# Performance work log

Measured on AMD Instinct MI355X. Metric: run time of the kernel, lower is better.

The kernel has to match this reference:

```python
import jax, jax.numpy as jnp
import numpy as np

V, H, E, B, T = 32000, 1024, 512, 32, 64
EPS = 1e-5


def setup_inputs() -> dict:
    key = jax.random.key(0)
    ks = jax.random.split(key, 12)
    s = 0.05
    return {
        'image_feat': jax.random.normal(ks[0], (B, 2048), jnp.float32),
        'captions': jax.random.randint(ks[1], (B, T), 0, V, jnp.int64)
            if jax.config.jax_enable_x64 else jax.random.randint(ks[1], (B, T), 0, V, jnp.int32),
        'lin_W': jax.random.normal(ks[2], (E, 2048), jnp.float32) * s,
        'lin_b': jnp.zeros((E,), jnp.float32),
        'bn_gamma': jnp.ones((E,), jnp.float32),
        'bn_beta': jnp.zeros((E,), jnp.float32),
        'emb': jax.random.normal(ks[3], (V, E), jnp.float32) * s,
        'lstm_Wih0': jax.random.normal(ks[4], (4 * H, E), jnp.float32) * s,
        'lstm_Whh0': jax.random.normal(ks[5], (4 * H, H), jnp.float32) * s,
        'lstm_bih0': jnp.zeros((4 * H,), jnp.float32),
        'lstm_bhh0': jnp.zeros((4 * H,), jnp.float32),
        'lstm_Wih1': jax.random.normal(ks[6], (4 * H, H), jnp.float32) * s,
        'lstm_Whh1': jax.random.normal(ks[7], (4 * H, H), jnp.float32) * s,
        'lstm_bih1': jnp.zeros((4 * H,), jnp.float32),
        'lstm_bhh1': jnp.zeros((4 * H,), jnp.float32),
        'fc_W': jax.random.normal(ks[8], (V, H), jnp.float32) * s,
        'fc_b': jnp.zeros((V,), jnp.float32),
    }


def _lstm_layer(xs, Wih, Whh, bih, bhh):
    # xs: (B, T, in) -> hs: (B, T, H). PyTorch gate order i,f,g,o.
    b, t, _ = xs.shape
    h_dim = Whh.shape[1]
    pre = jnp.einsum('bti,gi->btg', xs, Wih) + bih + bhh  # input part for all steps

    def step(carry, p):
        h, c = carry
        g = p + h @ Whh.T
        i, f, gg, o = jnp.split(g, 4, axis=-1)
        c = jax.nn.sigmoid(f) * c + jax.nn.sigmoid(i) * jnp.tanh(gg)
        h = jax.nn.sigmoid(o) * jnp.tanh(c)
        return (h, c), h

    h0 = jnp.zeros((b, h_dim), xs.dtype)
    (_, _), hs = jax.lax.scan(step, (h0, h0), jnp.swapaxes(pre, 0, 1))
    return jnp.swapaxes(hs, 0, 1)


def reference(image_feat, captions, lin_W, lin_b, bn_gamma, bn_beta, emb,
              lstm_Wih0, lstm_Whh0, lstm_bih0, lstm_bhh0,
              lstm_Wih1, lstm_Whh1, lstm_bih1, lstm_bhh1, fc_W, fc_b):
    # image embed: Linear + BatchNorm1d (training-mode batch stats)
    x = image_feat @ lin_W.T + lin_b  # (B, E)
    mu = jnp.mean(x, axis=0)
    var = jnp.var(x, axis=0)
    x = bn_gamma * (x - mu) * jax.lax.rsqrt(var + EPS) + bn_beta

    # teacher-forced decode: step0 = image embed, steps 1..T-1 = caption embeds
    cap_emb = emb[captions[:, :-1]]  # (B, T-1, E)
    xs = jnp.concatenate([x[:, None, :], cap_emb], axis=1)  # (B, T, E)

    hs = _lstm_layer(xs, lstm_Wih0, lstm_Whh0, lstm_bih0, lstm_bhh0)
    hs = _lstm_layer(hs, lstm_Wih1, lstm_Whh1, lstm_bih1, lstm_bhh1)

    return jnp.einsum('bth,vh->btv', hs, fc_W) + fc_b  # (B, T, V)
```

## Files before the change

### kernel.cpp

```cpp
#include <hip/hip_runtime.h>

typedef __bf16 bf16;
typedef __attribute__((ext_vector_type(4))) float floatx4;
typedef __attribute__((ext_vector_type(8))) bf16 bf16x8;
typedef __attribute__((ext_vector_type(4))) bf16 bf16x4;
typedef __attribute__((ext_vector_type(4))) unsigned uintx4;
typedef __attribute__((ext_vector_type(2))) unsigned uintx2;

typedef const __attribute__((address_space(1))) void gconst_t;
typedef __attribute__((address_space(3))) void lds_t;

__device__ __forceinline__ void load_lds16(const void* g, void* l) {
  __builtin_amdgcn_global_load_lds((gconst_t*)g, (lds_t*)l, 16, 0, 0);
}

__device__ __forceinline__ float sigm(float x) { return 1.f / (1.f + __expf(-x)); }
__device__ __forceinline__ float tanh_f(float x) { return 2.f / (1.f + __expf(-2.f * x)) - 1.f; }

__device__ __forceinline__ void st_coh_u32(void* p, unsigned v) {
  asm volatile("global_store_dword %0, %1, off sc0 sc1" :: "v"(p), "v"(v) : "memory");
}
__device__ __forceinline__ void st_coh_u128(void* p, uintx4 v) {
  asm volatile("global_store_dwordx4 %0, %1, off sc0 sc1" :: "v"(p), "v"(v) : "memory");
}
__device__ __forceinline__ uintx2 ld_coh_u32x2(const void* p) {
  uintx2 r;
  asm volatile("global_load_dwordx2 %0, %1, off sc0 sc1\n\ts_waitcnt vmcnt(0)"
               : "=v"(r) : "v"(p) : "memory");
  return r;
}

__global__ void k_cvt(const float* __restrict__ in, bf16* __restrict__ out, int n4) {
  int i = blockIdx.x * 256 + threadIdx.x;
  if (i < n4) {
    float4 v = ((const float4*)in)[i];
    bf16x4 u = { (bf16)v.x, (bf16)v.y, (bf16)v.z, (bf16)v.w };
    ((bf16x4*)out)[i] = u;
  }
}

__global__ void k_bias_sum(const float* __restrict__ a, const float* __restrict__ b,
                           float* __restrict__ o, int n) {
  int i = blockIdx.x * 256 + threadIdx.x;
  if (i < n) o[i] = a[i] + b[i];
}

__global__ void k_zero(unsigned* __restrict__ p) {
  p[threadIdx.x] = 0u;
}

__global__ __launch_bounds__(256) void k_linbn(
    const float* __restrict__ img, const float* __restrict__ W,
    const float* __restrict__ lb, const float* __restrict__ gamma,
    const float* __restrict__ beta, bf16* __restrict__ xs)
{
  const int e = blockIdx.x;
  const int wave = threadIdx.x >> 6, lane = threadIdx.x & 63;
  __shared__ float sums[32];
  const float* wrow = W + (size_t)e * 2048;
  for (int b = wave; b < 32; b += 4) {
    const float* irow = img + (size_t)b * 2048;
    float s = 0.f;
#pragma unroll
    for (int j = 0; j < 8; ++j) {
      const int k = j * 256 + lane * 4;
      float4 a = *(const float4*)(irow + k);
      float4 w = *(const float4*)(wrow + k);
      s += a.x * w.x + a.y * w.y + a.z * w.z + a.w * w.w;
    }
#pragma unroll
    for (int off = 32; off > 0; off >>= 1) s += __shfl_down(s, off);
    if (lane == 0) sums[b] = s + lb[e];
  }
  __syncthreads();
  if (threadIdx.x < 32) {
    const float x = sums[threadIdx.x];
    float m = x, m2 = x * x;
#pragma unroll
    for (int mask = 16; mask > 0; mask >>= 1) {
      m  += __shfl_xor(m, mask);
      m2 += __shfl_xor(m2, mask);
    }
    m *= (1.f / 32.f); m2 *= (1.f / 32.f);
    const float var = m2 - m * m;
    const float xn = gamma[e] * (x - m) * rsqrtf(var + 1e-5f) + beta[e];
    xs[(size_t)threadIdx.x * 64 * 512 + e] = (bf16)xn;
  }
}

__global__ void k_embed(const int* __restrict__ cap, const float* __restrict__ emb,
                        bf16* __restrict__ xs)
{
  const int blk = blockIdx.x;
  const int b = blk / 63, j = blk % 63;
  const int tok = cap[b * 64 + j];
  const float* src = emb + (size_t)tok * 512;
  bf16* dst = xs + ((size_t)b * 64 + j + 1) * 512;
  float4 v = ((const float4*)src)[threadIdx.x];
  bf16x4 u = { (bf16)v.x, (bf16)v.y, (bf16)v.z, (bf16)v.w };
  *(bf16x4*)(dst + threadIdx.x * 4) = u;
}

__global__ __launch_bounds__(256) void k_gemm(
    const bf16* __restrict__ A, const float* __restrict__ Bt,
    const float* __restrict__ bias, float* __restrict__ C,
    int K, int N)
{
  __shared__ bf16 lA[128 * 32];
  __shared__ bf16 lB[128 * 32];
  const int tid = threadIdx.x;
  const int lane = tid & 63;
  const int wm = ((tid >> 6) >> 1) * 64;
  const int wn = ((tid >> 6) & 1) * 64;
  const int nwg = gridDim.x * gridDim.y;
  int wg = blockIdx.y * gridDim.x + blockIdx.x;
  wg = (wg & 7) * (nwg >> 3) + (wg >> 3);
  const size_t row0 = (size_t)(wg & 15) * 128;
  const size_t col0 = (size_t)(wg >> 4) * 128;
  floatx4 acc[4][4] = {};
  const bf16*  aSrc = A  + (row0 + (tid >> 2)) * (size_t)K + (tid & 3) * 8;
  const float* bSrc = Bt + (col0 + (tid >> 3)) * (size_t)K + (tid & 7) * 4;
  char* lAb = (char*)&lA[0];

  for (int k0 = 0; k0 < K; k0 += 32) {
    __syncthreads();
#pragma unroll
    for (int s = 0; s < 2; ++s)
      load_lds16(aSrc + (size_t)s * 64 * K + k0, lAb + s * 4096 + tid * 16);
#pragma unroll
    for (int s = 0; s < 4; ++s) {
      float4 v = *(const float4*)(bSrc + (size_t)s * 32 * K + k0);
      bf16x4 u = { (bf16)v.x, (bf16)v.y, (bf16)v.z, (bf16)v.w };
      *(bf16x4*)&lB[(s * 32 + (tid >> 3)) * 32 + (tid & 7) * 4] = u;
    }
    __syncthreads();
    bf16x8 af[4], bfv[4];
#pragma unroll
    for (int i = 0; i < 4; ++i)
      af[i] = *(const bf16x8*)&lA[(wm + i * 16 + (lane & 15)) * 32 + (lane >> 4) * 8];
#pragma unroll
    for (int j = 0; j < 4; ++j)
      bfv[j] = *(const bf16x8*)&lB[(wn + j * 16 + (lane & 15)) * 32 + (lane >> 4) * 8];
#pragma unroll
    for (int i = 0; i < 4; ++i)
#pragma unroll
      for (int j = 0; j < 4; ++j)
        acc[i][j] = __builtin_amdgcn_mfma_f32_16x16x32_bf16(af[i], bfv[j], acc[i][j], 0, 0, 0);
  }
#pragma unroll
  for (int i = 0; i < 4; ++i)
#pragma unroll
    for (int j = 0; j < 4; ++j)
#pragma unroll
      for (int r = 0; r < 4; ++r) {
        const size_t row = row0 + wm + i * 16 + (lane >> 4) * 4 + r;
        const size_t col = col0 + wn + j * 16 + (lane & 15);
        C[row * (size_t)N + col] = acc[i][j][r] + bias[col];
      }
}

__global__ __launch_bounds__(256) void k_gemm_bf(
    const bf16* __restrict__ A, const bf16* __restrict__ B,
    const float* __restrict__ bias, float* __restrict__ C,
    int K, int N)
{
  __shared__ bf16 lA[128 * 32];
  __shared__ bf16 lB[128 * 32];
  const int tid = threadIdx.x;
  const int lane = tid & 63;
  const int wm = ((tid >> 6) >> 1) * 64;
  const int wn = ((tid >> 6) & 1) * 64;
  const int nwg = gridDim.x * gridDim.y;
  int wg = blockIdx.y * gridDim.x + blockIdx.x;
  wg = (wg & 7) * (nwg >> 3) + (wg >> 3);
  const size_t row0 = (size_t)(wg & 15) * 128;
  const size_t col0 = (size_t)(wg >> 4) * 128;
  floatx4 acc[4][4] = {};
  const bf16* aSrc = A + (row0 + (tid >> 2)) * (size_t)K + (tid & 3) * 8;
  const bf16* bSrc = B + (col0 + (tid >> 2)) * (size_t)K + (tid & 3) * 8;
  char* lAb = (char*)&lA[0];
  char* lBb = (char*)&lB[0];

  for (int k0 = 0; k0 < K; k0 += 32) {
    __syncthreads();
#pragma unroll
    for (int s = 0; s < 2; ++s) {
      load_lds16(aSrc + (size_t)s * 64 * K + k0, lAb + s * 4096 + tid * 16);
      load_lds16(bSrc + (size_t)s * 64 * K + k0, lBb + s * 4096 + tid * 16);
    }
    __syncthreads();
    bf16x8 af[4], bfv[4];
#pragma unroll
    for (int i = 0; i < 4; ++i)
      af[i] = *(const bf16x8*)&lA[(wm + i * 16 + (lane & 15)) * 32 + (lane >> 4) * 8];
#pragma unroll
    for (int j = 0; j < 4; ++j)
      bfv[j] = *(const bf16x8*)&lB[(wn + j * 16 + (lane & 15)) * 32 + (lane >> 4) * 8];
#pragma unroll
    for (int i = 0; i < 4; ++i)
#pragma unroll
      for (int j = 0; j < 4; ++j)
        acc[i][j] = __builtin_amdgcn_mfma_f32_16x16x32_bf16(af[i], bfv[j], acc[i][j], 0, 0, 0);
  }
#pragma unroll
  for (int i = 0; i < 4; ++i)
#pragma unroll
    for (int j = 0; j < 4; ++j)
#pragma unroll
      for (int r = 0; r < 4; ++r) {
        const size_t row = row0 + wm + i * 16 + (lane >> 4) * 4 + r;
        const size_t col = col0 + wn + j * 16 + (lane & 15);
        C[row * (size_t)N + col] = acc[i][j][r] + bias[col];
      }
}

__device__ __forceinline__ void wait_flags(const unsigned* flags, unsigned tgt) {
  const int lane = threadIdx.x & 63;
  const unsigned* p = flags + 2 * lane;
  int spins = 0;
  for (;;) {
    uintx2 f = ld_coh_u32x2(p);
    if (__all(f.x >= tgt && f.y >= tgt)) break;
    if (++spins > 50000) break;
    __builtin_amdgcn_s_sleep(1);
  }
  asm volatile("" ::: "memory");
}

__global__ __launch_bounds__(256) void k_lstm_scan(
    bf16* __restrict__ hs, const float* __restrict__ pre,
    const bf16* __restrict__ whh, unsigned* __restrict__ flags)
{
  __shared__ bf16 lW[32 * 1024];
  __shared__ bf16 hstage[32][8];
  const int tid  = threadIdx.x;
  const int lane = tid & 63;
  const int wave = tid >> 6;
  const int tn   = wave >> 1;
  const int tb   = wave & 1;
  const int n0   = blockIdx.x * 8;

#pragma unroll
  for (int it = 0; it < 16; ++it) {
    const int idx  = it * 256 + tid;
    const int r    = idx >> 7;
    const int c16  = idx & 127;
    const int grow = (r & 3) * 1024 + n0 + (r >> 2);
    const bf16x8 v = *(const bf16x8*)(whh + (size_t)grow * 1024 + c16 * 8);
    int byte = r * 2048 + c16 * 16;
    byte ^= (r & 7) << 4;
    *(bf16x8*)((char*)lW + byte) = v;
  }
  __syncthreads();

  const int arow  = tn * 16 + (lane & 15);
  const int axor  = (arow & 7) << 4;
  const int abase = arow * 2048 + (lane >> 4) * 16;
  const int brow  = tb * 16 + (lane & 15);
  const int cown  = tn * 4 + (lane >> 4);
  const char* lWb = (const char*)lW;

  float cstate = 0.f;
  const float* preb = pre + (size_t)brow * 64 * 4096 + (n0 + cown);
  const bf16* hr = hs + (size_t)brow * 65536 + (lane >> 4) * 8;
  bf16* hwrow = hs + (size_t)tid * 65536 + n0;

#pragma unroll 1
  for (int t = 0; t < 64; ++t) {
    const float* pp = preb + (size_t)t * 4096;
    float g0 = pp[0], g1 = pp[1024], g2 = pp[2048], g3 = pp[3072];
    if (t > 0) {
      if (wave == 0) wait_flags(flags, (unsigned)t);
      __syncthreads();
      const bf16* hp = hr + (size_t)(t - 1) * 1024;
      floatx4 acc0 = {}, acc1 = {};
#pragma unroll
      for (int kk = 0; kk < 32; kk += 2) {
        const bf16x8 a0 = *(const bf16x8*)(lWb + ((abase + kk * 64) ^ axor));
        const bf16x8 b0 = *(const bf16x8*)(hp + kk * 32);
        acc0 = __builtin_amdgcn_mfma_f32_16x16x32_bf16(a0, b0, acc0, 0, 0, 0);
        const bf16x8 a1 = *(const bf16x8*)(lWb + ((abase + kk * 64 + 64) ^ axor));
        const bf16x8 b1 = *(const bf16x8*)(hp + kk * 32 + 32);
        acc1 = __builtin_amdgcn_mfma_f32_16x16x32_bf16(a1, b1, acc1, 0, 0, 0);
      }
      g0 += acc0[0] + acc1[0];
      g1 += acc0[1] + acc1[1];
      g2 += acc0[2] + acc1[2];
      g3 += acc0[3] + acc1[3];
    }
    const float iv = sigm(g0), fv = sigm(g1), gv = tanh_f(g2), ov = sigm(g3);
    cstate = fv * cstate + iv * gv;
    hstage[brow][cown] = (bf16)(ov * tanh_f(cstate));
    __syncthreads();
    if (tid < 32) {
      const uintx4 hv = *(const uintx4*)&hstage[tid][0];
      st_coh_u128(hwrow + (size_t)t * 1024, hv);
      asm volatile("s_waitcnt vmcnt(0)" ::: "memory");
    }
    __syncthreads();
    if (tid == 0)
      st_coh_u32(flags + blockIdx.x, (unsigned)(t + 1));
  }
}

extern "C" void kernel_launch(void* const* d_in, const int* in_sizes, int n_in,
                              void* d_out, int out_size, void* d_ws, size_t ws_size,
                              hipStream_t stream)
{
  const float* image = (const float*)d_in[0];
  const int*   caps  = (const int*)d_in[1];
  const float* linW  = (const float*)d_in[2];
  const float* linb  = (const float*)d_in[3];
  const float* gamma = (const float*)d_in[4];
  const float* beta  = (const float*)d_in[5];
  const float* emb   = (const float*)d_in[6];
  const float* Wih0  = (const float*)d_in[7];
  const float* Whh0  = (const float*)d_in[8];
  const float* bih0  = (const float*)d_in[9];
  const float* bhh0  = (const float*)d_in[10];
  const float* Wih1  = (const float*)d_in[11];
  const float* Whh1  = (const float*)d_in[12];
  const float* bih1  = (const float*)d_in[13];
  const float* bhh1  = (const float*)d_in[14];
  const float* fcW   = (const float*)d_in[15];
  const float* fcb   = (const float*)d_in[16];
  float* out = (float*)d_out;

  char* ws = (char*)d_ws;
  size_t off = 0;
  auto alloc = [&](size_t bytes) {
    char* p = ws + off;
    off += (bytes + 255) & ~(size_t)255;
    return p;
  };
  bf16*  whh0b = (bf16*)alloc(4096ull * 1024 * 2);
  bf16*  whh1b = (bf16*)alloc(4096ull * 1024 * 2);
  bf16*  xsb   = (bf16*)alloc(2048ull * 512 * 2);
  bf16*  hs0b  = (bf16*)alloc(2048ull * 1024 * 2);
  bf16*  hs1b  = (bf16*)alloc(2048ull * 1024 * 2);
  float* pre   = (float*)alloc(2048ull * 4096 * 4);
  float* bsum0 = (float*)alloc(4096 * 4);
  float* bsum1 = (float*)alloc(4096 * 4);
  unsigned* flg = (unsigned*)alloc(1024);
  const bool big = ws_size >= ((size_t)127 << 20);
  bf16* fcwb = big ? (bf16*)alloc(32000ull * 1024 * 2) : (bf16*)0;

  k_zero<<<1, 256, 0, stream>>>(flg);
  k_cvt<<<4096, 256, 0, stream>>>(Whh0, whh0b, 4096 * 1024 / 4);
  k_cvt<<<4096, 256, 0, stream>>>(Whh1, whh1b, 4096 * 1024 / 4);
  if (big) k_cvt<<<32000, 256, 0, stream>>>(fcW, fcwb, 32000 * 1024 / 4);
  k_bias_sum<<<16, 256, 0, stream>>>(bih0, bhh0, bsum0, 4096);
  k_bias_sum<<<16, 256, 0, stream>>>(bih1, bhh1, bsum1, 4096);
  k_linbn<<<512, 256, 0, stream>>>(image, linW, linb, gamma, beta, xsb);
  k_embed<<<2016, 128, 0, stream>>>(caps, emb, xsb);

  k_gemm<<<dim3(16, 32), 256, 0, stream>>>(xsb, Wih0, bsum0, pre, 512, 4096);
  k_lstm_scan<<<128, 256, 0, stream>>>(hs0b, pre, whh0b, flg);
  k_gemm<<<dim3(16, 32), 256, 0, stream>>>(hs0b, Wih1, bsum1, pre, 1024, 4096);
  k_lstm_scan<<<128, 256, 0, stream>>>(hs1b, pre, whh1b, flg + 128);
  if (big)
    k_gemm_bf<<<dim3(16, 250), 256, 0, stream>>>(hs1b, fcwb, fcb, out, 1024, 32000);
  else
    k_gemm<<<dim3(16, 250), 256, 0, stream>>>(hs1b, fcW, fcb, out, 1024, 32000);

  (void)in_sizes; (void)n_in; (void)out_size; (void)ws_size;
}
```

Baseline: 1.476 ms.

## Fuse both LSTM layers into one wavefront-pipelined persistent kernel

Result: slower. 1.553 ms (+5.2%).

```diff
diff --git a/kernel.cpp b/kernel.cpp
--- a/kernel.cpp
+++ b/kernel.cpp
@@ -26,6 +26,12 @@
 __device__ __forceinline__ uintx2 ld_coh_u32x2(const void* p) {
   uintx2 r;
   asm volatile("global_load_dwordx2 %0, %1, off sc0 sc1\n\ts_waitcnt vmcnt(0)"
+               : "=v"(r) : "v"(p) : "memory");
+  return r;
+}
+__device__ __forceinline__ uintx4 ld_coh_u32x4(const void* p) {
+  uintx4 r;
+  asm volatile("global_load_dwordx4 %0, %1, off sc0 sc1\n\ts_waitcnt vmcnt(0)"
                : "=v"(r) : "v"(p) : "memory");
   return r;
 }
@@ -214,43 +220,83 @@
       }
 }
 
-__device__ __forceinline__ void wait_flags(const unsigned* flags, unsigned tgt) {
+__device__ __forceinline__ void stage_w(const bf16* __restrict__ w, int n0,
+                                        char* ldsbase, int tid) {
+#pragma unroll
+  for (int it = 0; it < 16; ++it) {
+    const int idx  = it * 256 + tid;
+    const int r    = idx >> 7;
+    const int c16  = idx & 127;
+    const int grow = (r & 3) * 1024 + n0 + (r >> 2);
+    const bf16x8 v = *(const bf16x8*)(w + (size_t)grow * 1024 + c16 * 8);
+    int byte = r * 2048 + c16 * 16;
+    byte ^= (r & 7) << 4;
+    *(bf16x8*)(ldsbase + byte) = v;
+  }
+}
+
+__device__ __forceinline__ void gemv_pass(const char* lWb, int abase, int axor,
+                                          const bf16* hp, floatx4& acc0, floatx4& acc1) {
+#pragma unroll
+  for (int g8 = 0; g8 < 4; ++g8) {
+    bf16x8 hb[8];
+#pragma unroll
+    for (int u = 0; u < 8; ++u)
+      hb[u] = *(const bf16x8*)(hp + (g8 * 8 + u) * 32);
+#pragma unroll
+    for (int u = 0; u < 8; ++u) {
+      const bf16x8 a = *(const bf16x8*)(lWb + ((abase + (g8 * 8 + u) * 64) ^ axor));
+      if (u & 1) acc1 = __builtin_amdgcn_mfma_f32_16x16x32_bf16(a, hb[u], acc1, 0, 0, 0);
+      else       acc0 = __builtin_amdgcn_mfma_f32_16x16x32_bf16(a, hb[u], acc0, 0, 0, 0);
+    }
+  }
+}
+
+__device__ __forceinline__ void poll128(const unsigned* flags, unsigned tgt) {
   const int lane = threadIdx.x & 63;
   const unsigned* p = flags + 2 * lane;
   int spins = 0;
   for (;;) {
     uintx2 f = ld_coh_u32x2(p);
     if (__all(f.x >= tgt && f.y >= tgt)) break;
-    if (++spins > 50000) break;
+    if (++spins > 20000) break;
     __builtin_amdgcn_s_sleep(1);
   }
   asm volatile("" ::: "memory");
 }
 
-__global__ __launch_bounds__(256) void k_lstm_scan(
-    bf16* __restrict__ hs, const float* __restrict__ pre,
-    const bf16* __restrict__ whh, unsigned* __restrict__ flags)
-{
-  __shared__ bf16 lW[32 * 1024];
+__device__ __forceinline__ void poll256(const unsigned* flags, unsigned tgt0, unsigned tgt1) {
+  const int lane = threadIdx.x & 63;
+  const unsigned tgt = (lane < 32) ? tgt0 : tgt1;
+  const unsigned* p = flags + 4 * lane;
+  int spins = 0;
+  for (;;) {
+    uintx4 f = ld_coh_u32x4(p);
+    if (__all(f.x >= tgt && f.y >= tgt && f.z >= tgt && f.w >= tgt)) break;
+    if (++spins > 20000) break;
+    __builtin_amdgcn_s_sleep(1);
+  }
+  asm volatile("" ::: "memory");
+}
+
+__global__ __launch_bounds__(256, 1) void k_lstm_fused(
+    bf16* __restrict__ hs0, bf16* __restrict__ hs1,
+    const float* __restrict__ pre0, const float* __restrict__ bs1,
+    const bf16* __restrict__ whh0, const bf16* __restrict__ whh1,
+    const bf16* __restrict__ wih1, unsigned* __restrict__ flags)
+{
+  __shared__ bf16 lW[2][32 * 1024];
   __shared__ bf16 hstage[32][8];
   const int tid  = threadIdx.x;
   const int lane = tid & 63;
   const int wave = tid >> 6;
-  const int tn   = wave >> 1;
-  const int tb   = wave & 1;
-  const int n0   = blockIdx.x * 8;
-
-#pragma unroll
-  for (int it = 0; it < 16; ++it) {
-    const int idx  = it * 256 + tid;
-    const int r    = idx >> 7;
-    const int c16  = idx & 127;
-    const int grow = (r & 3) * 1024 + n0 + (r >> 2);
-    const bf16x8 v = *(const bf16x8*)(whh + (size_t)grow * 1024 + c16 * 8);
-    int byte = r * 2048 + c16 * 16;
-    byte ^= (r & 7) << 4;
-    *(bf16x8*)((char*)lW + byte) = v;
-  }
+  const bool l1  = blockIdx.x >= 128;
+  const int blk  = l1 ? (int)blockIdx.x - 128 : (int)blockIdx.x;
+  const int n0   = blk * 8;
+  const int tn   = wave >> 1, tb = wave & 1;
+
+  stage_w(l1 ? whh1 : whh0, n0, (char*)&lW[0][0], tid);
+  if (l1) stage_w(wih1, n0, (char*)&lW[1][0], tid);
   __syncthreads();
 
   const int arow  = tn * 16 + (lane & 15);
@@ -258,35 +304,47 @@
   const int abase = arow * 2048 + (lane >> 4) * 16;
   const int brow  = tb * 16 + (lane & 15);
   const int cown  = tn * 4 + (lane >> 4);
-  const char* lWb = (const char*)lW;
+  const char* lWhh = (const char*)&lW[0][0];
+  const char* lWih = (const char*)&lW[1][0];
+
+  float b0g = 0.f, b1g = 0.f, b2g = 0.f, b3g = 0.f;
+  if (l1) {
+    b0g = bs1[0 * 1024 + n0 + cown];
+    b1g = bs1[1 * 1024 + n0 + cown];
+    b2g = bs1[2 * 1024 + n0 + cown];
+    b3g = bs1[3 * 1024 + n0 + cown];
+  }
+
+  bf16* hw = l1 ? hs1 : hs0;
+  bf16* hwrow = hw + (size_t)tid * 65536 + n0;
+  const bf16* hr_own = hw  + (size_t)brow * 65536 + (lane >> 4) * 8;
+  const bf16* hr_h0  = hs0 + (size_t)brow * 65536 + (lane >> 4) * 8;
+  const float* preb  = pre0 + (size_t)brow * 64 * 4096 + (n0 + cown);
+  unsigned* myflag = flags + (l1 ? 128 : 0) + blk;
 
   float cstate = 0.f;
-  const float* preb = pre + (size_t)brow * 64 * 4096 + (n0 + cown);
-  const bf16* hr = hs + (size_t)brow * 65536 + (lane >> 4) * 8;
-  bf16* hwrow = hs + (size_t)tid * 65536 + n0;
-
 #pragma unroll 1
   for (int t = 0; t < 64; ++t) {
-    const float* pp = preb + (size_t)t * 4096;
-    float g0 = pp[0], g1 = pp[1024], g2 = pp[2048], g3 = pp[3072];
-    if (t > 0) {
-      if (wave == 0) wait_flags(flags, (unsigned)t);
+    float g0, g1, g2, g3;
+    floatx4 acc0 = {}, acc1 = {};
+    if (!l1) {
+      const float* pp = preb + (size_t)t * 4096;
+      g0 = pp[0]; g1 = pp[1024]; g2 = pp[2048]; g3 = pp[3072];
+      if (t > 0) {
+        if (wave == 0) poll128(flags, (unsigned)t);
+        __syncthreads();
+        gemv_pass(lWhh, abase, axor, hr_own + (size_t)(t - 1) * 1024, acc0, acc1);
+      }
+      g0 += acc0[0] + acc1[0]; g1 += acc0[1] + acc1[1];
+      g2 += acc0[2] + acc1[2]; g3 += acc0[3] + acc1[3];
+    } else {
+      if (wave == 0) poll256(flags, (unsigned)(t + 1), (unsigned)t);
       __syncthreads();
-      const bf16* hp = hr + (size_t)(t - 1) * 1024;
-      floatx4 acc0 = {}, acc1 = {};
-#pragma unroll
-      for (int kk = 0; kk < 32; kk += 2) {
-        const bf16x8 a0 = *(const bf16x8*)(lWb + ((abase + kk * 64) ^ axor));
-        const bf16x8 b0 = *(const bf16x8*)(hp + kk * 32);
-        acc0 = __builtin_amdgcn_mfma_f32_16x16x32_bf16(a0, b0, acc0, 0, 0, 0);
-        const bf16x8 a1 = *(const bf16x8*)(lWb + ((abase + kk * 64 + 64) ^ axor));
-        const bf16x8 b1 = *(const bf16x8*)(hp + kk * 32 + 32);
-        acc1 = __builtin_amdgcn_mfma_f32_16x16x32_bf16(a1, b1, acc1, 0, 0, 0);
-      }
-      g0 += acc0[0] + acc1[0];
-      g1 += acc0[1] + acc1[1];
-      g2 += acc0[2] + acc1[2];
-      g3 += acc0[3] + acc1[3];
+      gemv_pass(lWih, abase, axor, hr_h0 + (size_t)t * 1024, acc0, acc1);
+      if (t > 0)
+        gemv_pass(lWhh, abase, axor, hr_own + (size_t)(t - 1) * 1024, acc0, acc1);
+      g0 = b0g + acc0[0] + acc1[0]; g1 = b1g + acc0[1] + acc1[1];
+      g2 = b2g + acc0[2] + acc1[2]; g3 = b3g + acc0[3] + acc1[3];
     }
     const float iv = sigm(g0), fv = sigm(g1), gv = tanh_f(g2), ov = sigm(g3);
     cstate = fv * cstate + iv * gv;
@@ -296,10 +354,8 @@
       const uintx4 hv = *(const uintx4*)&hstage[tid][0];
       st_coh_u128(hwrow + (size_t)t * 1024, hv);
       asm volatile("s_waitcnt vmcnt(0)" ::: "memory");
-    }
-    __syncthreads();
-    if (tid == 0)
-      st_coh_u32(flags + blockIdx.x, (unsigned)(t + 1));
+      if (tid == 0) st_coh_u32(myflag, (unsigned)(t + 1));
+    }
   }
 }
 
@@ -335,6 +391,7 @@
   };
   bf16*  whh0b = (bf16*)alloc(4096ull * 1024 * 2);
   bf16*  whh1b = (bf16*)alloc(4096ull * 1024 * 2);
+  bf16*  wih1b = (bf16*)alloc(4096ull * 1024 * 2);
   bf16*  xsb   = (bf16*)alloc(2048ull * 512 * 2);
   bf16*  hs0b  = (bf16*)alloc(2048ull * 1024 * 2);
   bf16*  hs1b  = (bf16*)alloc(2048ull * 1024 * 2);
@@ -342,12 +399,13 @@
   float* bsum0 = (float*)alloc(4096 * 4);
   float* bsum1 = (float*)alloc(4096 * 4);
   unsigned* flg = (unsigned*)alloc(1024);
-  const bool big = ws_size >= ((size_t)127 << 20);
+  const bool big = ws_size >= ((size_t)136 << 20);
   bf16* fcwb = big ? (bf16*)alloc(32000ull * 1024 * 2) : (bf16*)0;
 
   k_zero<<<1, 256, 0, stream>>>(flg);
   k_cvt<<<4096, 256, 0, stream>>>(Whh0, whh0b, 4096 * 1024 / 4);
   k_cvt<<<4096, 256, 0, stream>>>(Whh1, whh1b, 4096 * 1024 / 4);
+  k_cvt<<<4096, 256, 0, stream>>>(Wih1, wih1b, 4096 * 1024 / 4);
   if (big) k_cvt<<<32000, 256, 0, stream>>>(fcW, fcwb, 32000 * 1024 / 4);
   k_bias_sum<<<16, 256, 0, stream>>>(bih0, bhh0, bsum0, 4096);
   k_bias_sum<<<16, 256, 0, stream>>>(bih1, bhh1, bsum1, 4096);
@@ -355,9 +413,8 @@
   k_embed<<<2016, 128, 0, stream>>>(caps, emb, xsb);
 
   k_gemm<<<dim3(16, 32), 256, 0, stream>>>(xsb, Wih0, bsum0, pre, 512, 4096);
-  k_lstm_scan<<<128, 256, 0, stream>>>(hs0b, pre, whh0b, flg);
-  k_gemm<<<dim3(16, 32), 256, 0, stream>>>(hs0b, Wih1, bsum1, pre, 1024, 4096);
-  k_lstm_scan<<<128, 256, 0, stream>>>(hs1b, pre, whh1b, flg + 128);
+  k_lstm_fused<<<256, 256, 0, stream>>>(hs0b, hs1b, pre, bsum1,
+                                        whh0b, whh1b, wih1b, flg);
   if (big)
     k_gemm_bf<<<dim3(16, 250), 256, 0, stream>>>(hs1b, fcwb, fcb, out, 1024, 32000);
   else
```
